# Performance work log

Measured on AMD Instinct MI355X. Metric: run time of the kernel, lower is better.

## Reference

```python
import jax, jax.numpy as jnp
import numpy as np

B, S, H = 1, 4096, 3584
NQ, NKV, D = 16, 8, 256
N_REP = NQ // NKV  # GQA repeat factor = 2
WINDOW = 2048
SOFTCAP = 50.0
THETA = 10000.0
SCALE = D ** -0.5


def rotate_half(x):
    h = x.shape[-1] // 2
    return jnp.concatenate([-x[..., h:], x[..., :h]], axis=-1)


def setup_inputs() -> dict:
    key = jax.random.key(0)
    k0, k1, k2, k3, k4 = jax.random.split(key, 5)
    return {
        "hidden_states": jax.random.normal(k0, (B, S, H), jnp.float32),
        "wq": jax.random.normal(k1, (H, NQ * D), jnp.float32) / np.sqrt(H).astype(np.float32),
        "wk": jax.random.normal(k2, (H, NKV * D), jnp.float32) / np.sqrt(H).astype(np.float32),
        "wv": jax.random.normal(k3, (H, NKV * D), jnp.float32) / np.sqrt(H).astype(np.float32),
        "wo": jax.random.normal(k4, (NQ * D, H), jnp.float32) / np.sqrt(NQ * D).astype(np.float32),
        "position_ids": jnp.arange(S, dtype=jnp.int64 if jax.config.jax_enable_x64 else jnp.int32)[None, :],
    }


def reference(hidden_states, wq, wk, wv, wo, position_ids):
    b, s, h = hidden_states.shape
    # QKV projections (no bias, per attention_bias=False)
    q = (hidden_states @ wq).reshape(b, s, NQ, D).transpose(0, 2, 1, 3)   # [b, nq, s, d]
    k = (hidden_states @ wk).reshape(b, s, NKV, D).transpose(0, 2, 1, 3)  # [b, nkv, s, d]
    v = (hidden_states @ wv).reshape(b, s, NKV, D).transpose(0, 2, 1, 3)

    # Rotary embeddings (Gemma2RotaryEmbedding): freqs duplicated, rotate_half form
    pos = position_ids.astype(jnp.float32)                         # [b, s]
    inv_freq = 1.0 / (THETA ** (jnp.arange(0, D, 2, dtype=jnp.float32) / D))  # [d/2]
    freqs = pos[..., None] * inv_freq                              # [b, s, d/2]
    emb = jnp.concatenate([freqs, freqs], axis=-1)                 # [b, s, d]
    cos = jnp.cos(emb)[:, None, :, :]                              # [b, 1, s, d]
    sin = jnp.sin(emb)[:, None, :, :]
    q = q * cos + rotate_half(q) * sin
    k = k * cos + rotate_half(k) * sin

    # GQA: repeat_kv (repeat_interleave over head dim)
    k = jnp.repeat(k, N_REP, axis=1)  # [b, nq, s, d]
    v = jnp.repeat(v, N_REP, axis=1)

    # scaled scores + logit softcapping
    scores = jnp.einsum('bhqd,bhkd->bhqk', q, k) * SCALE
    scores = SOFTCAP * jnp.tanh(scores / SOFTCAP)

    # causal + sliding-window mask built from positions
    qpos = position_ids[:, None, :, None]  # [b,1,s,1]
    kpos = position_ids[:, None, None, :]  # [b,1,1,s]
    visible = (kpos <= qpos) & (kpos > qpos - WINDOW)
    scores = jnp.where(visible, scores, jnp.finfo(scores.dtype).min)

    attn = jax.nn.softmax(scores, axis=-1)
    out = jnp.einsum('bhqk,bhkd->bhqd', attn, v)      # [b, nq, s, d]
    out = out.transpose(0, 2, 1, 3).reshape(b, s, NQ * D)
    return out @ wo                                    # [b, s, h]
```

## Files before the change

kernel.cpp:

```cpp
#include <hip/hip_runtime.h>
#include <hip/hip_bf16.h>
#include <cstdint>
#include <cstddef>

#define DEVFN __device__ __forceinline__

typedef __attribute__((ext_vector_type(4))) float f32x4;
typedef __attribute__((ext_vector_type(8))) short bf16x8;
typedef __attribute__((ext_vector_type(4))) short short4v;

static constexpr int S = 4096;
static constexpr int H = 3584;
static constexpr int NQ = 16;
static constexpr int NKV = 8;
static constexpr int D = 256;
static constexpr int WINDOW = 2048;
static constexpr float SCALE = 0.0625f;

DEVFN unsigned short f2bf(float f) {
  union { float f; uint32_t u; } x; x.f = f;
  uint32_t u = x.u;
  u += 0x7fffu + ((u >> 16) & 1u);
  return (unsigned short)(u >> 16);
}
DEVFN float bf2f(unsigned short h) {
  union { uint32_t u; float f; } x; x.u = ((uint32_t)h) << 16;
  return x.f;
}

DEVFN void load_lds16(const void* g, void* l) {
  __builtin_amdgcn_global_load_lds((const __attribute__((address_space(1))) void*)g,
                                   (__attribute__((address_space(3))) void*)l,
                                   16, 0, 0);
}

__global__ __launch_bounds__(256) void cast_hs_kernel(const float* __restrict__ in,
                                                      unsigned short* __restrict__ out) {
  int i = (blockIdx.x * 256 + threadIdx.x) * 4;
  float4 v = *(const float4*)(in + i);
  short4v o;
  o[0] = (short)f2bf(v.x); o[1] = (short)f2bf(v.y);
  o[2] = (short)f2bf(v.z); o[3] = (short)f2bf(v.w);
  *(short4v*)(out + i) = o;
}

__global__ void transpose_cast_kernel(const float* __restrict__ in, unsigned short* __restrict__ out,
                                      int rows, int cols, int out_ld) {
  __shared__ float tile[32][33];
  int r0 = blockIdx.y * 32, c0 = blockIdx.x * 32;
  int tx = threadIdx.x, ty = threadIdx.y;
#pragma unroll
  for (int j = 0; j < 32; j += 8)
    tile[ty + j][tx] = in[(size_t)(r0 + ty + j) * cols + (c0 + tx)];
  __syncthreads();
#pragma unroll
  for (int j = 0; j < 32; j += 8)
    out[(size_t)(c0 + ty + j) * out_ld + (r0 + tx)] = f2bf(tile[tx][ty + j]);
}

__global__ __launch_bounds__(256) void rope_table_kernel(float* __restrict__ cs) {
  int idx = blockIdx.x * 256 + threadIdx.x;
  int s = idx >> 7, i = idx & 127;
  float inv = 1.0f / powf(10000.0f, (float)i * (1.0f / 128.0f));
  float f = (float)s * inv;
  cs[idx] = cosf(f);
  cs[(S * 128) + idx] = sinf(f);
}

__global__ __launch_bounds__(256) void rope_apply_kernel(unsigned short* __restrict__ q,
                                                         unsigned short* __restrict__ k,
                                                         const float* __restrict__ cs) {
  int idx = blockIdx.x * 256 + threadIdx.x;
  int i4 = (idx & 31) * 4;
  int s = (idx >> 5) & (S - 1);
  int hh = idx >> 17;
  unsigned short* base = (hh < NQ) ? (q + ((size_t)hh * S + s) * D)
                                   : (k + ((size_t)(hh - NQ) * S + s) * D);
  float4 c  = *(const float4*)(cs + (s << 7) + i4);
  float4 sn = *(const float4*)(cs + (S * 128) + (s << 7) + i4);
  short4v a = *(short4v*)(base + i4);
  short4v b = *(short4v*)(base + i4 + 128);
  short4v o1, o2;
  o1[0] = (short)f2bf(bf2f((unsigned short)a[0]) * c.x - bf2f((unsigned short)b[0]) * sn.x);
  o1[1] = (short)f2bf(bf2f((unsigned short)a[1]) * c.y - bf2f((unsigned short)b[1]) * sn.y);
  o1[2] = (short)f2bf(bf2f((unsigned short)a[2]) * c.z - bf2f((unsigned short)b[2]) * sn.z);
  o1[3] = (short)f2bf(bf2f((unsigned short)a[3]) * c.w - bf2f((unsigned short)b[3]) * sn.w);
  o2[0] = (short)f2bf(bf2f((unsigned short)b[0]) * c.x + bf2f((unsigned short)a[0]) * sn.x);
  o2[1] = (short)f2bf(bf2f((unsigned short)b[1]) * c.y + bf2f((unsigned short)a[1]) * sn.y);
  o2[2] = (short)f2bf(bf2f((unsigned short)b[2]) * c.z + bf2f((unsigned short)a[2]) * sn.z);
  o2[3] = (short)f2bf(bf2f((unsigned short)b[3]) * c.w + bf2f((unsigned short)a[3]) * sn.w);
  *(short4v*)(base + i4) = o1;
  *(short4v*)(base + i4 + 128) = o2;
}

DEVFN void gemm256_mainloop(const unsigned short* __restrict__ A,
                            const unsigned short* __restrict__ Bt,
                            int Kdim, int lda, int ldb, int row0, int col0,
                            char* lds, f32x4 acc[8][4]) {
  const int tid = threadIdx.x, lane = tid & 63;
  const int w = tid >> 6;
  const int wm = w >> 2, wn = w & 3;
  const int NT = Kdim >> 6;

  const int u = ((tid & 7) * 16) ^ (((tid >> 3) & 7) << 4);
  const int srow = (tid >> 3) + (u >> 6) * 128;
  const int sc = (u & 63) >> 1;

  const unsigned short* aSrc = A + (size_t)(row0 + srow) * lda + sc;
  const unsigned short* bSrc = Bt + (size_t)(col0 + srow) * ldb + sc;
  const size_t aj = (size_t)64 * lda, bj = (size_t)64 * ldb;

  char* const dA = lds + tid * 16;
  char* const dB = lds + 32768 + tid * 16;

  const int aoff = (lane & 15) * 128 + ((((lane >> 4) * 16) + wm * 64) ^ ((lane & 7) << 4));
  const int boff = ((wn & 1) * 64 + (lane & 15)) * 128 +
                   ((((lane >> 4) * 16) + (wn >> 1) * 64) ^ ((lane & 7) << 4));

#define STAGE_A(kt2, kh) do { \
    char* d_ = dA + (((kt2) & 1) << 16) + ((kh) << 14); \
    const unsigned short* s_ = aSrc + (kt2) * 64 + (kh) * 32; \
    load_lds16(s_, d_); load_lds16(s_ + aj, d_ + 8192); } while (0)
#define STAGE_B(kt2, kh) do { \
    char* d_ = dB + (((kt2) & 1) << 16) + ((kh) << 14); \
    const unsigned short* s_ = bSrc + (kt2) * 64 + (kh) * 32; \
    load_lds16(s_, d_); load_lds16(s_ + bj, d_ + 8192); } while (0)

  STAGE_A(0, 0); STAGE_B(0, 0); STAGE_A(0, 1); STAGE_B(0, 1);
  if (NT > 1) { STAGE_A(1, 0); STAGE_B(1, 0); }
  asm volatile("s_waitcnt vmcnt(4)" ::: "memory");
  __builtin_amdgcn_s_barrier();
  asm volatile("" ::: "memory");

  for (int kt = 0; kt < NT; ++kt) {
    const char* lA = lds + ((kt & 1) << 16) + aoff;
    const char* lB = lds + ((kt & 1) << 16) + 32768 + boff;
    bf16x8 bfr[4];
#pragma unroll
    for (int ph = 0; ph < 4; ++ph) {
      const int kh = ph >> 1;
      const int mh = ph & 1;
      bf16x8 af[4];
#pragma unroll
      for (int j = 0; j < 4; ++j)
        af[j] = *(const bf16x8*)(lA + (kh << 14) + (mh * 4 + j) * 2048);
      if (mh == 0) {
#pragma unroll
        for (int n = 0; n < 4; ++n)
          bfr[n] = *(const bf16x8*)(lB + (kh << 14) + n * 2048);
      }
      if (ph == 0)      { if (kt + 1 < NT) STAGE_A(kt + 1, 1); }
      else if (ph == 1) { if (kt + 1 < NT) STAGE_B(kt + 1, 1); }
      else if (ph == 2) { if (kt + 2 < NT) STAGE_A(kt + 2, 0); }
      else              { if (kt + 2 < NT) STAGE_B(kt + 2, 0); }

      asm volatile("" ::: "memory");
      __builtin_amdgcn_s_barrier();
      asm volatile("" ::: "memory");
      __builtin_amdgcn_s_setprio(1);
#pragma unroll
      for (int j = 0; j < 4; ++j)
#pragma unroll
        for (int n = 0; n < 4; ++n)
          acc[mh * 4 + j][n] =
              __builtin_amdgcn_mfma_f32_16x16x32_bf16(af[j], bfr[n], acc[mh * 4 + j][n], 0, 0, 0);
      __builtin_amdgcn_s_setprio(0);
      if (ph == 3) {
        if (kt < NT - 2) asm volatile("s_waitcnt vmcnt(4)" ::: "memory");
        else             asm volatile("s_waitcnt vmcnt(0)" ::: "memory");
      }
      asm volatile("" ::: "memory");
      __builtin_amdgcn_s_barrier();
      asm volatile("" ::: "memory");
    }
  }
#undef STAGE_A
#undef STAGE_B
}

__global__ __launch_bounds__(512, 2) void gemm_qkv_kernel(const unsigned short* __restrict__ A,
                                                          const unsigned short* __restrict__ Bt,
                                                          unsigned short* __restrict__ qb,
                                                          unsigned short* __restrict__ kbuf,
                                                          unsigned short* __restrict__ vtb) {
  extern __shared__ char lds[];
  int bid = blockIdx.x;
  bid = (bid & 7) * 64 + (bid >> 3);
  const int bx = bid & 15, by = bid >> 4;
  const int row0 = bx * 256, col0 = by * 256;
  f32x4 acc[8][4];
  f32x4 z = {0.f, 0.f, 0.f, 0.f};
#pragma unroll
  for (int m = 0; m < 8; ++m)
#pragma unroll
    for (int n = 0; n < 4; ++n) acc[m][n] = z;

  gemm256_mainloop(A, Bt, H, H, H, row0, col0, lds, acc);

  const int lane = threadIdx.x & 63, w = threadIdx.x >> 6;
  const int wm = w >> 2, wn = w & 3;
  const int rbase = row0 + wm * 128 + (lane >> 4) * 4;
  const int cbase = col0 + wn * 64 + (lane & 15);
  if (col0 < 4096) {
#pragma unroll
    for (int m = 0; m < 8; ++m)
#pragma unroll
      for (int n = 0; n < 4; ++n)
#pragma unroll
        for (int r = 0; r < 4; ++r) {
          int row = rbase + m * 16 + r;
          int col = cbase + n * 16;
          qb[((size_t)(col >> 8) * S + row) * D + (col & 255)] = f2bf(acc[m][n][r]);
        }
  } else if (col0 < 6144) {
#pragma unroll
    for (int m = 0; m < 8; ++m)
#pragma unroll
      for (int n = 0; n < 4; ++n)
#pragma unroll
        for (int r = 0; r < 4; ++r) {
          int row = rbase + m * 16 + r;
          int c2 = cbase + n * 16 - 4096;
          kbuf[((size_t)(c2 >> 8) * S + row) * D + (c2 & 255)] = f2bf(acc[m][n][r]);
        }
  } else {
#pragma unroll
    for (int m = 0; m < 8; ++m)
#pragma unroll
      for (int n = 0; n < 4; ++n)
#pragma unroll
        for (int r = 0; r < 4; ++r) {
          int row = rbase + m * 16 + r;
          int c3 = cbase + n * 16 - 6144;
          vtb[((size_t)(c3 >> 8) * D + (c3 & 255)) * S + row] = f2bf(acc[m][n][r]);
        }
  }
}

__global__ __launch_bounds__(512, 2) void gemm_out_kernel(const unsigned short* __restrict__ A,
                                                          const unsigned short* __restrict__ Bt,
                                                          float* __restrict__ C) {
  extern __shared__ char lds[];
  int bid = blockIdx.x;
  bid = (bid & 7) * 28 + (bid >> 3);
  const int bx = bid & 15, by = bid >> 4;
  const int row0 = bx * 256, col0 = by * 256;
  f32x4 acc[8][4];
  f32x4 z = {0.f, 0.f, 0.f, 0.f};
#pragma unroll
  for (int m = 0; m < 8; ++m)
#pragma unroll
    for (int n = 0; n < 4; ++n) acc[m][n] = z;

  gemm256_mainloop(A, Bt, NQ * D, NQ * D, NQ * D, row0, col0, lds, acc);

  const int lane = threadIdx.x & 63, w = threadIdx.x >> 6;
  const int wm = w >> 2, wn = w & 3;
  const int rbase = row0 + wm * 128 + (lane >> 4) * 4;
  const int cbase = col0 + wn * 64 + (lane & 15);
#pragma unroll
  for (int m = 0; m < 8; ++m)
#pragma unroll
    for (int n = 0; n < 4; ++n)
#pragma unroll
      for (int r = 0; r < 4; ++r)
        C[(size_t)(rbase + m * 16 + r) * H + cbase + n * 16] = acc[m][n][r];
}

__global__ __launch_bounds__(256, 2) void attn_kernel(const unsigned short* __restrict__ q,
                                                      const unsigned short* __restrict__ kk_,
                                                      const unsigned short* __restrict__ vt,
                                                      unsigned short* __restrict__ aout) {
  __shared__ __align__(16) char kl[2][16384];
  __shared__ __align__(16) char vl[2][16384];
  __shared__ __align__(16) char pl[8192];
  const int tid = threadIdx.x, lane = tid & 63, w = tid >> 6;
  const int h = blockIdx.y, hv = h >> 1;
  const int q0 = blockIdx.x * 128;
  const int ql = lane & 15;
  const int grp = lane >> 4;
  const int qw = q0 + w * 32;

  bf16x8 qf[2][8];
#pragma unroll
  for (int qs = 0; qs < 2; ++qs) {
    const unsigned short* qrow = q + ((size_t)h * S + qw + qs * 16 + ql) * D;
#pragma unroll
    for (int t = 0; t < 8; ++t)
      qf[qs][t] = *(const bf16x8*)(qrow + t * 32 + grp * 8);
  }

  f32x4 oacc[2][16];
  f32x4 z = {0.f, 0.f, 0.f, 0.f};
#pragma unroll
  for (int qs = 0; qs < 2; ++qs)
#pragma unroll
    for (int i = 0; i < 16; ++i) oacc[qs][i] = z;
  float lrun[2] = {0.0f, 0.0f};

  int lo = q0 - (WINDOW - 1); if (lo < 0) lo = 0;
  const int kb0 = lo & ~31;
  const int kend = q0 + 96;

  const unsigned short* kbase = kk_ + (size_t)hv * S * D;
  const unsigned short* vbase = vt + (size_t)hv * D * S;
  int koff[4], voff[4];
#pragma unroll
  for (int j = 0; j < 4; ++j) {
    int c = w + 4 * j;
    int key = c * 2 + (lane >> 5);
    int colK = (((lane & 31) * 16) ^ ((key & 7) << 4)) >> 1;
    koff[j] = key * D + colK;
    int dd = c * 16 + (lane >> 2);
    int colV = (((lane & 3) * 16) ^ (((dd >> 1) & 3) << 4)) >> 1;
    voff[j] = dd * S + colV;
  }

  auto stage = [&](int buf, int kb) {
#pragma unroll
    for (int j = 0; j < 4; ++j) {
      int c = w + 4 * j;
      load_lds16(kbase + (size_t)kb * D + koff[j], &kl[buf][c * 1024]);
      load_lds16(vbase + kb + voff[j], &vl[buf][c * 1024]);
    }
  };

  stage(0, kb0);
  int cur = 0;
  const int psw = ((ql >> 1) & 3) << 4;
  char* pw = pl + w * 2048;
  const int ksw = (ql & 7) << 4;

  for (int kb = kb0; kb <= kend; kb += 32) {
    __syncthreads();
    if (kb + 32 <= kend) stage(cur ^ 1, kb + 32);

    f32x4 sacc[2][2];
    sacc[0][0] = z; sacc[0][1] = z; sacc[1][0] = z; sacc[1][1] = z;
#pragma unroll
    for (int t = 0; t < 8; ++t) {
      bf16x8 af[2];
#pragma unroll
      for (int ms = 0; ms < 2; ++ms)
        af[ms] = *(const bf16x8*)(kl[cur] + (ms * 16 + ql) * 512 + ((t * 64 + grp * 16) ^ ksw));
#pragma unroll
      for (int qs = 0; qs < 2; ++qs)
#pragma unroll
        for (int ms = 0; ms < 2; ++ms)
          sacc[qs][ms] = __builtin_amdgcn_mfma_f32_16x16x32_bf16(af[ms], qf[qs][t], sacc[qs][ms], 0, 0, 0);
    }

#pragma unroll
    for (int qs = 0; qs < 2; ++qs) {
      const int qsb = qw + qs * 16;
      const int qg = qsb + ql;
      float pv[8];
#pragma unroll
      for (int i = 0; i < 8; ++i) {
        float x = sacc[qs][i >> 2][i & 3];
        float e = __expf(x * (SCALE / 25.0f));
        float rc = __builtin_amdgcn_rcpf(e + 1.0f);
        pv[i] = __expf(rc * -100.0f);
      }
      if (kb + 31 > qsb) {
#pragma unroll
        for (int i = 0; i < 8; ++i) {
          int key = kb + (i >> 2) * 16 + grp * 4 + (i & 3);
          if (key > qg) pv[i] = 0.0f;
        }
      } else if (kb < qsb - 2032) {
#pragma unroll
        for (int i = 0; i < 8; ++i) {
          int key = kb + (i >> 2) * 16 + grp * 4 + (i & 3);
          if (key <= qg - WINDOW) pv[i] = 0.0f;
        }
      }
#pragma unroll
      for (int i = 0; i < 8; ++i) lrun[qs] += pv[i];

#pragma unroll
      for (int ms = 0; ms < 2; ++ms) {
        short4v pk;
        pk[0] = (short)f2bf(pv[ms * 4 + 0]);
        pk[1] = (short)f2bf(pv[ms * 4 + 1]);
        pk[2] = (short)f2bf(pv[ms * 4 + 2]);
        pk[3] = (short)f2bf(pv[ms * 4 + 3]);
        *(short4v*)(pw + (qs * 16 + ql) * 64 + ((ms * 32 + grp * 8) ^ psw)) = pk;
      }
    }
    asm volatile("s_waitcnt lgkmcnt(0)" ::: "memory");
    bf16x8 pb[2];
#pragma unroll
    for (int qs = 0; qs < 2; ++qs)
      pb[qs] = *(const bf16x8*)(pw + (qs * 16 + ql) * 64 + ((grp * 16) ^ psw));

#pragma unroll
    for (int nt = 0; nt < 16; ++nt) {
      int dr = nt * 16 + ql;
      bf16x8 va = *(const bf16x8*)(vl[cur] + dr * 64 + ((grp * 16) ^ (((dr >> 1) & 3) << 4)));
      oacc[0][nt] = __builtin_amdgcn_mfma_f32_16x16x32_bf16(va, pb[0], oacc[0][nt], 0, 0, 0);
      oacc[1][nt] = __builtin_amdgcn_mfma_f32_16x16x32_bf16(va, pb[1], oacc[1][nt], 0, 0, 0);
    }
    cur ^= 1;
  }

#pragma unroll
  for (int qs = 0; qs < 2; ++qs) {
    float l = lrun[qs];
    l += __shfl_xor(l, 16);
    l += __shfl_xor(l, 32);
    l = fmaxf(l, 1e-35f);
    float rl = 1.0f / l;
    unsigned short* orow = aout + (size_t)(qw + qs * 16 + ql) * (NQ * D) + h * D;
#pragma unroll
    for (int nt = 0; nt < 16; ++nt) {
      short4v o;
      o[0] = (short)f2bf(oacc[qs][nt][0] * rl);
      o[1] = (short)f2bf(oacc[qs][nt][1] * rl);
      o[2] = (short)f2bf(oacc[qs][nt][2] * rl);
      o[3] = (short)f2bf(oacc[qs][nt][3] * rl);
      *(short4v*)(orow + nt * 16 + grp * 4) = o;
    }
  }
}

extern "C" void kernel_launch(void* const* d_in, const int* in_sizes, int n_in,
                              void* d_out, int out_size, void* d_ws, size_t ws_size,
                              hipStream_t stream) {
  const float* hs = (const float*)d_in[0];
  const float* wq = (const float*)d_in[1];
  const float* wk = (const float*)d_in[2];
  const float* wv = (const float*)d_in[3];
  const float* wo = (const float*)d_in[4];
  float* out = (float*)d_out;

  char* ws = (char*)d_ws;
  size_t off = 0;
  auto alloc = [&](size_t bytes) {
    char* p = ws + off;
    off += (bytes + 255) & ~(size_t)255;
    return p;
  };
  unsigned short* hsb   = (unsigned short*)alloc((size_t)S * H * 2);
  unsigned short* wqkvT = (unsigned short*)alloc((size_t)8192 * H * 2);
  unsigned short* woT   = (unsigned short*)alloc((size_t)H * 4096 * 2);
  unsigned short* qb    = (unsigned short*)alloc((size_t)NQ * S * D * 2);
  unsigned short* kbuf  = (unsigned short*)alloc((size_t)NKV * S * D * 2);
  unsigned short* vtb   = (unsigned short*)alloc((size_t)NKV * D * S * 2);
  unsigned short* aob   = (unsigned short*)alloc((size_t)S * NQ * D * 2);
  float*          cs    = (float*)alloc((size_t)S * 128 * 2 * 4);
  if (off > ws_size) return;

  dim3 tb(32, 8);
  cast_hs_kernel<<<(S * H) / 1024, 256, 0, stream>>>(hs, hsb);
  transpose_cast_kernel<<<dim3(4096 / 32, H / 32), tb, 0, stream>>>(wq, wqkvT, H, 4096, H);
  transpose_cast_kernel<<<dim3(2048 / 32, H / 32), tb, 0, stream>>>(wk, wqkvT + (size_t)4096 * H, H, 2048, H);
  transpose_cast_kernel<<<dim3(2048 / 32, H / 32), tb, 0, stream>>>(wv, wqkvT + (size_t)6144 * H, H, 2048, H);
  transpose_cast_kernel<<<dim3(H / 32, 4096 / 32), tb, 0, stream>>>(wo, woT, 4096, H, 4096);
  rope_table_kernel<<<(S * 128) / 256, 256, 0, stream>>>(cs);
  gemm_qkv_kernel<<<512, 512, 131072, stream>>>(hsb, wqkvT, qb, kbuf, vtb);
  rope_apply_kernel<<<((NQ + NKV) * S * 32) / 256, 256, 0, stream>>>(qb, kbuf, cs);
  attn_kernel<<<dim3(S / 128, NQ), 256, 0, stream>>>(qb, kbuf, vtb, aob);
  gemm_out_kernel<<<224, 512, 131072, stream>>>(aob, woT, out);
}
```

Before: 621.9 us.

## Fuse RoPE into QKV GEMM epilogue and vectorize cast/transpose kernels

```diff
diff --git a/kernel.cpp b/kernel.cpp
--- a/kernel.cpp
+++ b/kernel.cpp
@@ -8,6 +8,7 @@
 typedef __attribute__((ext_vector_type(4))) float f32x4;
 typedef __attribute__((ext_vector_type(8))) short bf16x8;
 typedef __attribute__((ext_vector_type(4))) short short4v;
+typedef __attribute__((ext_vector_type(8))) short short8v;
 
 static constexpr int S = 4096;
 static constexpr int H = 3584;
@@ -18,10 +19,8 @@
 static constexpr float SCALE = 0.0625f;
 
 DEVFN unsigned short f2bf(float f) {
-  union { float f; uint32_t u; } x; x.f = f;
-  uint32_t u = x.u;
-  u += 0x7fffu + ((u >> 16) & 1u);
-  return (unsigned short)(u >> 16);
+  __hip_bfloat16 h = __float2bfloat16(f);
+  return __builtin_bit_cast(unsigned short, h);
 }
 DEVFN float bf2f(unsigned short h) {
   union { uint32_t u; float f; } x; x.u = ((uint32_t)h) << 16;
@@ -36,61 +35,51 @@
 
 __global__ __launch_bounds__(256) void cast_hs_kernel(const float* __restrict__ in,
                                                       unsigned short* __restrict__ out) {
-  int i = (blockIdx.x * 256 + threadIdx.x) * 4;
-  float4 v = *(const float4*)(in + i);
-  short4v o;
-  o[0] = (short)f2bf(v.x); o[1] = (short)f2bf(v.y);
-  o[2] = (short)f2bf(v.z); o[3] = (short)f2bf(v.w);
-  *(short4v*)(out + i) = o;
-}
-
-__global__ void transpose_cast_kernel(const float* __restrict__ in, unsigned short* __restrict__ out,
-                                      int rows, int cols, int out_ld) {
-  __shared__ float tile[32][33];
-  int r0 = blockIdx.y * 32, c0 = blockIdx.x * 32;
-  int tx = threadIdx.x, ty = threadIdx.y;
-#pragma unroll
-  for (int j = 0; j < 32; j += 8)
-    tile[ty + j][tx] = in[(size_t)(r0 + ty + j) * cols + (c0 + tx)];
+  int i = (blockIdx.x * 256 + threadIdx.x) * 8;
+  float4 a = *(const float4*)(in + i);
+  float4 b = *(const float4*)(in + i + 4);
+  short8v o;
+  o[0] = (short)f2bf(a.x); o[1] = (short)f2bf(a.y);
+  o[2] = (short)f2bf(a.z); o[3] = (short)f2bf(a.w);
+  o[4] = (short)f2bf(b.x); o[5] = (short)f2bf(b.y);
+  o[6] = (short)f2bf(b.z); o[7] = (short)f2bf(b.w);
+  *(short8v*)(out + i) = o;
+}
+
+__global__ __launch_bounds__(256) void transpose_cast_kernel(const float* __restrict__ in,
+                                                             unsigned short* __restrict__ out,
+                                                             int rows, int cols, int out_ld) {
+  __shared__ float tile[64][65];
+  const int r0 = blockIdx.y * 64, c0 = blockIdx.x * 64;
+  const int t = threadIdx.x;
+  const int rr = t >> 4, c4 = (t & 15) * 4;
+#pragma unroll
+  for (int j = 0; j < 4; ++j) {
+    float4 v = *(const float4*)(in + (size_t)(r0 + rr + j * 16) * cols + c0 + c4);
+    tile[rr + j * 16][c4 + 0] = v.x;
+    tile[rr + j * 16][c4 + 1] = v.y;
+    tile[rr + j * 16][c4 + 2] = v.z;
+    tile[rr + j * 16][c4 + 3] = v.w;
+  }
   __syncthreads();
-#pragma unroll
-  for (int j = 0; j < 32; j += 8)
-    out[(size_t)(c0 + ty + j) * out_ld + (r0 + tx)] = f2bf(tile[tx][ty + j]);
+  const int c = t >> 2, ch = (t & 3) * 16;
+  short8v o0, o1;
+#pragma unroll
+  for (int j = 0; j < 8; ++j) o0[j] = (short)f2bf(tile[ch + j][c]);
+#pragma unroll
+  for (int j = 0; j < 8; ++j) o1[j] = (short)f2bf(tile[ch + 8 + j][c]);
+  unsigned short* dst = out + (size_t)(c0 + c) * out_ld + r0 + ch;
+  *(short8v*)dst = o0;
+  *(short8v*)(dst + 8) = o1;
 }
 
 __global__ __launch_bounds__(256) void rope_table_kernel(float* __restrict__ cs) {
   int idx = blockIdx.x * 256 + threadIdx.x;
   int s = idx >> 7, i = idx & 127;
-  float inv = 1.0f / powf(10000.0f, (float)i * (1.0f / 128.0f));
+  float inv = exp2f((float)i * -0.10381025296523007f);
   float f = (float)s * inv;
   cs[idx] = cosf(f);
   cs[(S * 128) + idx] = sinf(f);
-}
-
-__global__ __launch_bounds__(256) void rope_apply_kernel(unsigned short* __restrict__ q,
-                                                         unsigned short* __restrict__ k,
-                                                         const float* __restrict__ cs) {
-  int idx = blockIdx.x * 256 + threadIdx.x;
-  int i4 = (idx & 31) * 4;
-  int s = (idx >> 5) & (S - 1);
-  int hh = idx >> 17;
-  unsigned short* base = (hh < NQ) ? (q + ((size_t)hh * S + s) * D)
-                                   : (k + ((size_t)(hh - NQ) * S + s) * D);
-  float4 c  = *(const float4*)(cs + (s << 7) + i4);
-  float4 sn = *(const float4*)(cs + (S * 128) + (s << 7) + i4);
-  short4v a = *(short4v*)(base + i4);
-  short4v b = *(short4v*)(base + i4 + 128);
-  short4v o1, o2;
-  o1[0] = (short)f2bf(bf2f((unsigned short)a[0]) * c.x - bf2f((unsigned short)b[0]) * sn.x);
-  o1[1] = (short)f2bf(bf2f((unsigned short)a[1]) * c.y - bf2f((unsigned short)b[1]) * sn.y);
-  o1[2] = (short)f2bf(bf2f((unsigned short)a[2]) * c.z - bf2f((unsigned short)b[2]) * sn.z);
-  o1[3] = (short)f2bf(bf2f((unsigned short)a[3]) * c.w - bf2f((unsigned short)b[3]) * sn.w);
-  o2[0] = (short)f2bf(bf2f((unsigned short)b[0]) * c.x + bf2f((unsigned short)a[0]) * sn.x);
-  o2[1] = (short)f2bf(bf2f((unsigned short)b[1]) * c.y + bf2f((unsigned short)a[1]) * sn.y);
-  o2[2] = (short)f2bf(bf2f((unsigned short)b[2]) * c.z + bf2f((unsigned short)a[2]) * sn.z);
-  o2[3] = (short)f2bf(bf2f((unsigned short)b[3]) * c.w + bf2f((unsigned short)a[3]) * sn.w);
-  *(short4v*)(base + i4) = o1;
-  *(short4v*)(base + i4 + 128) = o2;
 }
 
 DEVFN void gemm256_mainloop(const unsigned short* __restrict__ A,
@@ -180,6 +169,7 @@
 
 __global__ __launch_bounds__(512, 2) void gemm_qkv_kernel(const unsigned short* __restrict__ A,
                                                           const unsigned short* __restrict__ Bt,
+                                                          const float* __restrict__ cs,
                                                           unsigned short* __restrict__ qb,
                                                           unsigned short* __restrict__ kbuf,
                                                           unsigned short* __restrict__ vtb) {
@@ -201,28 +191,40 @@
   const int wm = w >> 2, wn = w & 3;
   const int rbase = row0 + wm * 128 + (lane >> 4) * 4;
   const int cbase = col0 + wn * 64 + (lane & 15);
-  if (col0 < 4096) {
-#pragma unroll
-    for (int m = 0; m < 8; ++m)
+
+  if (col0 < 6144) {
+    const bool isQ = (col0 < 4096);
+    const float sgn = (wn < 2) ? -1.0f : 1.0f;
+    float* lf = (float*)lds;
+    const float* pp = lf + (((w ^ 2) << 6) + lane) * 16;
+#pragma unroll
+    for (int m = 0; m < 8; ++m) {
+      __syncthreads();
 #pragma unroll
       for (int n = 0; n < 4; ++n)
 #pragma unroll
+        for (int r = 0; r < 4; ++r)
+          lf[threadIdx.x * 16 + n * 4 + r] = acc[m][n][r];
+      __syncthreads();
+#pragma unroll
+      for (int n = 0; n < 4; ++n) {
+        const int dm = (wn & 1) * 64 + n * 16 + (lane & 15);
+#pragma unroll
         for (int r = 0; r < 4; ++r) {
-          int row = rbase + m * 16 + r;
-          int col = cbase + n * 16;
-          qb[((size_t)(col >> 8) * S + row) * D + (col & 255)] = f2bf(acc[m][n][r]);
+          const int row = rbase + m * 16 + r;
+          const float c = cs[(row << 7) + dm];
+          const float s = cs[(S << 7) + (row << 7) + dm];
+          const float v = acc[m][n][r] * c + sgn * pp[n * 4 + r] * s;
+          const int col = cbase + n * 16;
+          if (isQ) {
+            qb[((size_t)(col >> 8) * S + row) * D + (col & 255)] = f2bf(v);
+          } else {
+            const int c2 = col - 4096;
+            kbuf[((size_t)(c2 >> 8) * S + row) * D + (c2 & 255)] = f2bf(v);
+          }
         }
-  } else if (col0 < 6144) {
-#pragma unroll
-    for (int m = 0; m < 8; ++m)
-#pragma unroll
-      for (int n = 0; n < 4; ++n)
-#pragma unroll
-        for (int r = 0; r < 4; ++r) {
-          int row = rbase + m * 16 + r;
-          int c2 = cbase + n * 16 - 4096;
-          kbuf[((size_t)(c2 >> 8) * S + row) * D + (c2 & 255)] = f2bf(acc[m][n][r]);
-        }
+      }
+    }
   } else {
 #pragma unroll
     for (int m = 0; m < 8; ++m)
@@ -357,10 +359,11 @@
       float pv[8];
 #pragma unroll
       for (int i = 0; i < 8; ++i) {
-        float x = sacc[qs][i >> 2][i & 3];
-        float e = __expf(x * (SCALE / 25.0f));
-        float rc = __builtin_amdgcn_rcpf(e + 1.0f);
-        pv[i] = __expf(rc * -100.0f);
+        float y = sacc[qs][i >> 2][i & 3] * (SCALE / 50.0f);
+        float y2 = y * y;
+        float t = y * (15.0f + y2) * __builtin_amdgcn_rcpf(15.0f + 6.0f * y2);
+        t = fminf(fmaxf(t, -1.0f), 1.0f);
+        pv[i] = __expf(50.0f * t - 50.0f);
       }
       if (kb + 31 > qsb) {
 #pragma unroll
@@ -451,15 +454,13 @@
   float*          cs    = (float*)alloc((size_t)S * 128 * 2 * 4);
   if (off > ws_size) return;
 
-  dim3 tb(32, 8);
-  cast_hs_kernel<<<(S * H) / 1024, 256, 0, stream>>>(hs, hsb);
-  transpose_cast_kernel<<<dim3(4096 / 32, H / 32), tb, 0, stream>>>(wq, wqkvT, H, 4096, H);
-  transpose_cast_kernel<<<dim3(2048 / 32, H / 32), tb, 0, stream>>>(wk, wqkvT + (size_t)4096 * H, H, 2048, H);
-  transpose_cast_kernel<<<dim3(2048 / 32, H / 32), tb, 0, stream>>>(wv, wqkvT + (size_t)6144 * H, H, 2048, H);
-  transpose_cast_kernel<<<dim3(H / 32, 4096 / 32), tb, 0, stream>>>(wo, woT, 4096, H, 4096);
+  cast_hs_kernel<<<(S * H) / 2048, 256, 0, stream>>>(hs, hsb);
+  transpose_cast_kernel<<<dim3(4096 / 64, H / 64), 256, 0, stream>>>(wq, wqkvT, H, 4096, H);
+  transpose_cast_kernel<<<dim3(2048 / 64, H / 64), 256, 0, stream>>>(wk, wqkvT + (size_t)4096 * H, H, 2048, H);
+  transpose_cast_kernel<<<dim3(2048 / 64, H / 64), 256, 0, stream>>>(wv, wqkvT + (size_t)6144 * H, H, 2048, H);
+  transpose_cast_kernel<<<dim3(H / 64, 4096 / 64), 256, 0, stream>>>(wo, woT, 4096, H, 4096);
   rope_table_kernel<<<(S * 128) / 256, 256, 0, stream>>>(cs);
-  gemm_qkv_kernel<<<512, 512, 131072, stream>>>(hsb, wqkvT, qb, kbuf, vtb);
-  rope_apply_kernel<<<((NQ + NKV) * S * 32) / 256, 256, 0, stream>>>(qb, kbuf, cs);
+  gemm_qkv_kernel<<<512, 512, 131072, stream>>>(hsb, wqkvT, cs, qb, kbuf, vtb);
   attn_kernel<<<dim3(S / 128, NQ), 256, 0, stream>>>(qb, kbuf, vtb, aob);
   gemm_out_kernel<<<224, 512, 131072, stream>>>(aob, woT, out);
 }
```

Measured after the change: 676.0 us. 1.09x slower.
